# Optimization experiments

Measured on AMD Instinct MI355X. Metric: run time of the kernel, lower is better.

The kernel has to match this reference:

```python
import jax, jax.numpy as jnp
import numpy as np

HIDDEN = 2048
H = 16            # num heads
Q_RANK = 1536
KV_RANK = 512
D_NOPE = 128
D_ROPE = 64
D_QK = D_NOPE + D_ROPE   # 192
D_V = 128
ROPE_BASE = 10000.0
EPS = 1e-6


def _rms_norm(x, w):
    xf = x.astype(jnp.float32)
    var = jnp.mean(xf * xf, axis=-1, keepdims=True)
    return w * (xf * jax.lax.rsqrt(var + EPS)).astype(x.dtype)


def _rotate_half(x):
    x1, x2 = x[..., : x.shape[-1] // 2], x[..., x.shape[-1] // 2:]
    return jnp.concatenate((-x2, x1), axis=-1)


def _rope_cos_sin(position_ids, dtype):
    inv_freq = 1.0 / (ROPE_BASE ** (jnp.arange(0, D_ROPE, 2, dtype=jnp.float32) / D_ROPE))
    freqs = position_ids.astype(jnp.float32)[..., None] * inv_freq  # [b,s,32]
    emb = jnp.concatenate((freqs, freqs), axis=-1)                  # [b,s,64]
    return jnp.cos(emb).astype(dtype), jnp.sin(emb).astype(dtype)


def setup_inputs() -> dict:
    key = jax.random.key(0)
    ks = jax.random.split(key, 8)
    b, s = 1, 2048
    scale = 0.02
    return {
        "hidden_states": jax.random.normal(ks[0], (b, s, HIDDEN), jnp.float32),
        "position_ids": jnp.broadcast_to(jnp.arange(s, dtype=jnp.int64)[None, :], (b, s)),
        "q_a_w": jax.random.normal(ks[1], (Q_RANK, HIDDEN), jnp.float32) * scale,
        "q_a_ln_w": jnp.ones((Q_RANK,), jnp.float32),
        "q_b_w": jax.random.normal(ks[2], (H * D_QK, Q_RANK), jnp.float32) * scale,
        "kv_a_w": jax.random.normal(ks[3], (KV_RANK + D_ROPE, HIDDEN), jnp.float32) * scale,
        "kv_a_ln_w": jnp.ones((KV_RANK,), jnp.float32),
        "kv_b_w": jax.random.normal(ks[4], (H * (D_NOPE + D_V), KV_RANK), jnp.float32) * scale,
        "o_w": jax.random.normal(ks[5], (HIDDEN, H * D_V), jnp.float32) * scale,
    }


def reference(hidden_states, position_ids, q_a_w, q_a_ln_w, q_b_w, kv_a_w, kv_a_ln_w, kv_b_w, o_w):
    b, s, _ = hidden_states.shape
    softmax_scale = D_QK ** (-0.5)

    # Q path: low-rank down-proj -> RMSNorm -> up-proj
    q_a = hidden_states @ q_a_w.T                              # [b,s,q_rank]
    q = (_rms_norm(q_a, q_a_ln_w) @ q_b_w.T).reshape(b, s, H, D_QK)
    q_nope, q_pe = q[..., :D_NOPE], q[..., D_NOPE:]

    # KV path: joint down-proj -> split latent / rope part
    kv_a = hidden_states @ kv_a_w.T                            # [b,s,kv_rank+rope]
    compressed_kv = _rms_norm(kv_a[..., :KV_RANK], kv_a_ln_w)  # [b,s,kv_rank]
    k_pe = kv_a[..., KV_RANK:]                                 # [b,s,rope]
    kv_b = (compressed_kv @ kv_b_w.T).reshape(b, s, H, D_NOPE + D_V)
    k_nope, v = kv_b[..., :D_NOPE], kv_b[..., D_NOPE:]

    # decoupled RoPE on the rope slice
    cos, sin = _rope_cos_sin(position_ids, hidden_states.dtype)  # [b,s,64]
    cos, sin = cos[:, :, None, :], sin[:, :, None, :]            # [b,s,1,64]
    q_pe = q_pe * cos + _rotate_half(q_pe) * sin                 # [b,s,H,64]
    k_pe_h = jnp.broadcast_to(k_pe[:, :, None, :], (b, s, H, D_ROPE))
    k_pe_h = k_pe_h * cos + _rotate_half(k_pe_h) * sin

    q_full = jnp.concatenate([q_nope, q_pe], axis=-1)            # [b,s,H,192]
    k_full = jnp.concatenate([k_nope, k_pe_h], axis=-1)          # [b,s,H,192]

    # naive materialized attention (matches reference)
    scores = jnp.einsum("bqhd,bkhd->bhqk", q_full, k_full) * softmax_scale
    causal = jnp.triu(jnp.full((s, s), -jnp.inf, dtype=scores.dtype), k=1)
    scores = scores + causal
    probs = jax.nn.softmax(scores.astype(jnp.float32), axis=-1).astype(q_full.dtype)
    attn = jnp.einsum("bhqk,bkhd->bqhd", probs, v).reshape(b, s, H * D_V)
    return attn @ o_w.T
```

## Files before the change

kernel.cpp:

```cpp
#include <hip/hip_runtime.h>
#include <stdint.h>

#define S_LEN 2048
#define HIDDEN_ 2048
#define NH 16
#define QR 1536
#define KVR 512
#define DN 128
#define DR 64
#define DQK 192
#define DV 128

typedef __attribute__((ext_vector_type(8))) short bf16x8;
typedef __attribute__((ext_vector_type(4))) float f32x4;
typedef __attribute__((ext_vector_type(4))) unsigned short u16x4;
typedef unsigned short u16;
typedef unsigned int u32;

#define GLOAD_LDS16(g, l)                                                      \
    __builtin_amdgcn_global_load_lds(                                          \
        (const __attribute__((address_space(1))) void*)(g),                    \
        (__attribute__((address_space(3))) void*)(l), 16, 0, 0)

__device__ inline float bf2f(u16 x) {
    union { u32 u; float f; } v; v.u = ((u32)x) << 16; return v.f;
}
__device__ inline u16 f2bf(float f) {
    union { float f; u32 u; } v; v.f = f;
    u32 u = v.u;
    return (u16)((u + 0x7fffu + ((u >> 16) & 1u)) >> 16);
}

__global__ void cvt_multi(const float* s0, u16* d0, int n0,
                          const float* s1, u16* d1, int n1,
                          const float* s2, u16* d2, int n2,
                          const float* s3, u16* d3, int n3,
                          const float* s4, u16* d4, int n4,
                          const float* s5, u16* d5, int n5)
{
    const float* src; u16* dst; int n;
    switch (blockIdx.y) {
        case 0: src = s0; dst = d0; n = n0; break;
        case 1: src = s1; dst = d1; n = n1; break;
        case 2: src = s2; dst = d2; n = n2; break;
        case 3: src = s3; dst = d3; n = n3; break;
        case 4: src = s4; dst = d4; n = n4; break;
        default: src = s5; dst = d5; n = n5; break;
    }
    int i = (blockIdx.x * 256 + threadIdx.x) * 4;
    if (i + 3 < n) {
        float4 v = *(const float4*)(src + i);
        dst[i + 0] = f2bf(v.x);
        dst[i + 1] = f2bf(v.y);
        dst[i + 2] = f2bf(v.z);
        dst[i + 3] = f2bf(v.w);
    }
}

__global__ __launch_bounds__(256, 3)
void gemm_bt(const u16* __restrict__ A, const u16* __restrict__ B,
             void* __restrict__ Cv, int M, int N, int K, int out_f32)
{
    __shared__ u16 sA[128 * 32];
    __shared__ u16 sB[128 * 32];
    const int tid  = threadIdx.x;
    const int wave = tid >> 6;
    const int lane = tid & 63;
    const int l16  = lane & 15;
    const int quad = lane >> 4;
    const int m_blk = blockIdx.y * 128;
    const int n_blk = blockIdx.x * 128;
    const int wm = (wave >> 1) * 64;
    const int wn = (wave & 1) * 64;

    const f32x4 zero4 = {0.f, 0.f, 0.f, 0.f};
    f32x4 acc[4][4];
#pragma unroll
    for (int i = 0; i < 4; i++)
#pragma unroll
        for (int j = 0; j < 4; j++) acc[i][j] = zero4;

    const int srow = lane >> 2;
    const int scol = (lane & 3) * 8;

    for (int k0 = 0; k0 < K; k0 += 32) {
        __syncthreads();
#pragma unroll
        for (int p = 0; p < 2; p++) {
            const int rbase = wave * 32 + p * 16;
            const int row = rbase + srow;
            const u16* ga = A + (size_t)(m_blk + row) * K + k0 + scol;
            GLOAD_LDS16(ga, &sA[rbase * 32]);
            int brow = n_blk + row; if (brow >= N) brow = N - 1;
            const u16* gb = B + (size_t)brow * K + k0 + scol;
            GLOAD_LDS16(gb, &sB[rbase * 32]);
        }
        __syncthreads();

        bf16x8 af[4], bfr[4];
#pragma unroll
        for (int i = 0; i < 4; i++)
            af[i] = *(const bf16x8*)(sA + (wm + i * 16 + l16) * 32 + quad * 8);
#pragma unroll
        for (int j = 0; j < 4; j++)
            bfr[j] = *(const bf16x8*)(sB + (wn + j * 16 + l16) * 32 + quad * 8);
#pragma unroll
        for (int i = 0; i < 4; i++)
#pragma unroll
            for (int j = 0; j < 4; j++)
                acc[i][j] = __builtin_amdgcn_mfma_f32_16x16x32_bf16(
                    af[i], bfr[j], acc[i][j], 0, 0, 0);
    }

#pragma unroll
    for (int i = 0; i < 4; i++)
#pragma unroll
        for (int j = 0; j < 4; j++)
#pragma unroll
            for (int r = 0; r < 4; r++) {
                int mrow = m_blk + wm + i * 16 + quad * 4 + r;
                int ncol = n_blk + wn + j * 16 + l16;
                if (ncol < N) {
                    if (out_f32)
                        ((float*)Cv)[(size_t)mrow * N + ncol] = acc[i][j][r];
                    else
                        ((u16*)Cv)[(size_t)mrow * N + ncol] = f2bf(acc[i][j][r]);
                }
            }
}

__global__ void rmsnorm2_k(const u16* __restrict__ X0, const float* __restrict__ W0,
                           u16* __restrict__ Y0,
                           const u16* __restrict__ X1, const float* __restrict__ W1,
                           u16* __restrict__ Y1, int in_stride)
{
    const u16* X; const float* W; u16* Y; int len, out_stride;
    if (blockIdx.y == 0) { X = X0; W = W0; Y = Y0; len = QR;  out_stride = QR; }
    else                 { X = X1; W = W1; Y = Y1; len = KVR; out_stride = KVR; }
    const int row = blockIdx.x;
    const u16* x = X + (size_t)row * in_stride;
    u16* y = Y + (size_t)row * out_stride;
    float ss = 0.f;
    for (int i = threadIdx.x; i < len; i += 256) { float v = bf2f(x[i]); ss += v * v; }
#pragma unroll
    for (int off = 32; off; off >>= 1) ss += __shfl_down(ss, off, 64);
    __shared__ float red[4];
    if ((threadIdx.x & 63) == 0) red[threadIdx.x >> 6] = ss;
    __syncthreads();
    float tot = red[0] + red[1] + red[2] + red[3];
    float inv = 1.0f / sqrtf(tot / (float)len + 1e-6f);
    for (int i = threadIdx.x; i < len; i += 256)
        y[i] = f2bf(W[i] * bf2f(x[i]) * inv);
}

__global__ void rope_repack(const u16* __restrict__ q,
                            const u16* __restrict__ kvb,
                            const u16* __restrict__ kva_pe,
                            int kva_stride,
                            u16* __restrict__ Q, u16* __restrict__ Kf)
{
    const int s = blockIdx.x;
    const float pos = (float)s;
    const int t = threadIdx.x;
    __shared__ float cs[64], sn[64];
    __shared__ u16 kpe_r[64];
    if (t < 64) {
        int jf = t & 31;
        float freq = powf(10000.f, -(float)(2 * jf) / 64.f);
        float ang = pos * freq;
        cs[t] = cosf(ang);
        sn[t] = sinf(ang);
    }
    __syncthreads();
    if (t < 64) {
        int j = t;
        float x = bf2f(kva_pe[(size_t)s * kva_stride + j]);
        float other = (j < 32) ? -bf2f(kva_pe[(size_t)s * kva_stride + j + 32])
                               :  bf2f(kva_pe[(size_t)s * kva_stride + j - 32]);
        kpe_r[j] = f2bf(x * cs[j] + other * sn[j]);
    }
    __syncthreads();

    for (int idx = t; idx < NH * DQK; idx += 256) {
        int h = idx / DQK, d = idx % DQK;
        const size_t qrow = (size_t)s * (NH * DQK) + h * DQK;
        u16 qv;
        if (d < DN) qv = q[qrow + d];
        else {
            int j = d - DN;
            float x = bf2f(q[qrow + DN + j]);
            float other = (j < 32) ? -bf2f(q[qrow + DN + j + 32])
                                   :  bf2f(q[qrow + DN + j - 32]);
            qv = f2bf(x * cs[j] + other * sn[j]);
        }
        Q[((size_t)h * S_LEN + s) * DQK + d] = qv;
        u16 kv;
        if (d < DN) kv = kvb[(size_t)s * (NH * 256) + h * 256 + d];
        else        kv = kpe_r[d - DN];
        Kf[((size_t)h * S_LEN + s) * DQK + d] = kv;
    }
}

__global__ void transpose_v(const u16* __restrict__ kvb, u16* __restrict__ Vt)
{
    __shared__ u16 tile[64][72];
    const int h  = blockIdx.z;
    const int s0 = blockIdx.x * 64;
    const int d0 = blockIdx.y * 64;
    const int t  = threadIdx.x;
#pragma unroll
    for (int p = 0; p < 2; p++) {
        int c = p * 256 + t;
        int r = c >> 3, col = (c & 7) * 8;
        *(bf16x8*)&tile[r][col] =
            *(const bf16x8*)&kvb[(size_t)(s0 + r) * (NH * 256) + h * 256 + 128 + d0 + col];
    }
    __syncthreads();
#pragma unroll
    for (int p = 0; p < 2; p++) {
        int c = p * 256 + t;
        int dr = c >> 3, sc = (c & 7) * 8;
        bf16x8 v;
#pragma unroll
        for (int j = 0; j < 8; j++) v[j] = (short)tile[sc + j][dr];
        *(bf16x8*)&Vt[((size_t)h * DV + d0 + dr) * S_LEN + s0 + sc] = v;
    }
}

__global__ __launch_bounds__(256, 2)
void mla_attn(const u16* __restrict__ Q, const u16* __restrict__ Kf,
              const u16* __restrict__ Vt, u16* __restrict__ attn)
{
    const int h     = blockIdx.y;
    const int strip = (h < 8) ? blockIdx.x : (31 - blockIdx.x);
    const int wave  = threadIdx.x >> 6;
    const int lane  = threadIdx.x & 63;
    const int l16   = lane & 15;
    const int quad  = lane >> 4;
    const int q0    = strip * 64 + wave * 16;
    const int qrow  = q0 + l16;

    const u16* Qh  = Q  + (size_t)h * S_LEN * DQK;
    const u16* Kh  = Kf + (size_t)h * S_LEN * DQK;
    const u16* Vth = Vt + (size_t)h * DV * S_LEN;

    __shared__ u16 sK[2][24 * 32 * 8];
    __shared__ u16 sV[2][4 * 128 * 8];
    __shared__ u16 pbuf[4][16][36];
    u16 (*pb)[36] = pbuf[wave];

    bf16x8 qf[6];
#pragma unroll
    for (int st = 0; st < 6; st++)
        qf[st] = *(const bf16x8*)(Qh + (size_t)qrow * DQK + st * 32 + quad * 8);

    const f32x4 zero4 = {0.f, 0.f, 0.f, 0.f};
    f32x4 oacc[8];
#pragma unroll
    for (int t = 0; t < 8; t++) oacc[t] = zero4;
    float mrow = -INFINITY, lrow = 0.f;

    const float scale = 0.07216878364870323f;
    const int T = 2 * strip + 2;

    auto stage = [&](int buf, int c0) {
#pragma unroll
        for (int g = 0; g < 3; g++) {
            int c = g * 256 + wave * 64 + lane;
            int row = c & 31, cg = c >> 5;
            GLOAD_LDS16(Kh + (size_t)(c0 + row) * DQK + cg * 8,
                        &sK[buf][(g * 256 + wave * 64) * 8]);
        }
#pragma unroll
        for (int g = 0; g < 2; g++) {
            int c = g * 256 + wave * 64 + lane;
            int d = c & 127, cg = c >> 7;
            GLOAD_LDS16(Vth + (size_t)d * S_LEN + c0 + cg * 8,
                        &sV[buf][(g * 256 + wave * 64) * 8]);
        }
    };

    stage(0, 0);

    for (int kt = 0; kt < T; kt++) {
        const int c0  = kt * 32;
        const int cur = kt & 1;
        __syncthreads();
        if (kt + 1 < T) stage(cur ^ 1, c0 + 32);

        if (c0 <= q0 + 15) {
            f32x4 s0 = zero4, s1 = zero4;
#pragma unroll
            for (int st = 0; st < 6; st++) {
                bf16x8 k0 = *(const bf16x8*)&sK[cur][((st * 4 + quad) * 32 + l16) * 8];
                bf16x8 k1 = *(const bf16x8*)&sK[cur][((st * 4 + quad) * 32 + 16 + l16) * 8];
                s0 = __builtin_amdgcn_mfma_f32_16x16x32_bf16(k0, qf[st], s0, 0, 0, 0);
                s1 = __builtin_amdgcn_mfma_f32_16x16x32_bf16(k1, qf[st], s1, 0, 0, 0);
            }
            bf16x8 vfr[8];
#pragma unroll
            for (int t = 0; t < 8; t++)
                vfr[t] = *(const bf16x8*)&sV[cur][(quad * 128 + t * 16 + l16) * 8];

            const bool full = (c0 + 31 <= q0);
            float v0[4], v1[4];
#pragma unroll
            for (int r = 0; r < 4; r++) {
                v0[r] = s0[r] * scale;
                v1[r] = s1[r] * scale;
                if (!full) {
                    if (c0 + quad * 4 + r > qrow)      v0[r] = -INFINITY;
                    if (c0 + 16 + quad * 4 + r > qrow) v1[r] = -INFINITY;
                }
            }
            float lm = fmaxf(fmaxf(fmaxf(v0[0], v0[1]), fmaxf(v0[2], v0[3])),
                             fmaxf(fmaxf(v1[0], v1[1]), fmaxf(v1[2], v1[3])));
            lm = fmaxf(lm, __shfl_xor(lm, 16, 64));
            lm = fmaxf(lm, __shfl_xor(lm, 32, 64));
            const float mnew  = fmaxf(mrow, lm);
            const float alpha = __expf(mrow - mnew);
            float p0[4], p1[4], rs = 0.f;
#pragma unroll
            for (int r = 0; r < 4; r++) {
                p0[r] = __expf(v0[r] - mnew);
                p1[r] = __expf(v1[r] - mnew);
                rs += p0[r] + p1[r];
            }
            rs += __shfl_xor(rs, 16, 64);
            rs += __shfl_xor(rs, 32, 64);
            lrow = lrow * alpha + rs;
            mrow = mnew;
#pragma unroll
            for (int t = 0; t < 8; t++) oacc[t] *= alpha;

            u16x4 pk0, pk1;
#pragma unroll
            for (int r = 0; r < 4; r++) { pk0[r] = f2bf(p0[r]); pk1[r] = f2bf(p1[r]); }
            *(u16x4*)&pb[l16][quad * 4]      = pk0;
            *(u16x4*)&pb[l16][16 + quad * 4] = pk1;
            asm volatile("s_waitcnt lgkmcnt(0)" ::: "memory");
            bf16x8 pfrag = *(const bf16x8*)(&pb[l16][quad * 8]);

#pragma unroll
            for (int t = 0; t < 8; t++)
                oacc[t] = __builtin_amdgcn_mfma_f32_16x16x32_bf16(vfr[t], pfrag,
                                                                  oacc[t], 0, 0, 0);
        }
    }

    const float linv = 1.0f / lrow;
#pragma unroll
    for (int t = 0; t < 8; t++) {
        u16x4 ov;
#pragma unroll
        for (int r = 0; r < 4; r++) ov[r] = f2bf(oacc[t][r] * linv);
        *(u16x4*)&attn[(size_t)qrow * (NH * DV) + h * DV + t * 16 + quad * 4] = ov;
    }
}

extern "C" void kernel_launch(void* const* d_in, const int* in_sizes, int n_in,
                              void* d_out, int out_size, void* d_ws, size_t ws_size,
                              hipStream_t stream)
{
    const float* hid      = (const float*)d_in[0];
    const float* q_a_w    = (const float*)d_in[2];
    const float* q_a_ln_w = (const float*)d_in[3];
    const float* q_b_w    = (const float*)d_in[4];
    const float* kv_a_w   = (const float*)d_in[5];
    const float* kv_a_ln_w= (const float*)d_in[6];
    const float* kv_b_w   = (const float*)d_in[7];
    const float* o_w      = (const float*)d_in[8];

    const int NQKV = QR + KVR + DR;

    char* base = (char*)d_ws;
    u16* qkvaw_b = (u16*)(base + 0);
    u16* qbw_b   = (u16*)(base + 8650752);
    u16* kvbw_b  = (u16*)(base + 18087936);
    u16* ow_b    = (u16*)(base + 22282240);
    u16* hid_b   = (u16*)(base + 30670848);
    u16* qkv_a   = (u16*)(base + 39059456);
    u16* q_n     = (u16*)(base + 47710208);
    u16* ckv     = (u16*)(base + 54001664);
    u16* qb      = (u16*)(base + 56098816);
    u16* kvb     = (u16*)(base + 68681728);
    u16* Qb      = (u16*)(base + 85458944);
    u16* Kb      = (u16*)(base + 98041856);
    u16* Vtb     = (u16*)(base + 110624768);
    u16* attnb   = (u16*)(base + 39059456);

    cvt_multi<<<dim3(4608, 6), 256, 0, stream>>>(
        hid,    hid_b,                          HIDDEN_ * S_LEN,
        q_a_w,  qkvaw_b,                        QR * HIDDEN_,
        kv_a_w, qkvaw_b + (size_t)QR * HIDDEN_, (KVR + DR) * HIDDEN_,
        q_b_w,  qbw_b,                          NH * DQK * QR,
        kv_b_w, kvbw_b,                         NH * 256 * KVR,
        o_w,    ow_b,                           HIDDEN_ * NH * DV);

    gemm_bt<<<dim3((NQKV + 127) / 128, S_LEN / 128), 256, 0, stream>>>(
        hid_b, qkvaw_b, qkv_a, S_LEN, NQKV, HIDDEN_, 0);
    rmsnorm2_k<<<dim3(S_LEN, 2), 256, 0, stream>>>(
        qkv_a, q_a_ln_w, q_n, qkv_a + QR, kv_a_ln_w, ckv, NQKV);
    gemm_bt<<<dim3(NH * DQK / 128, S_LEN / 128), 256, 0, stream>>>(
        q_n, qbw_b, qb, S_LEN, NH * DQK, QR, 0);
    gemm_bt<<<dim3(NH * 256 / 128, S_LEN / 128), 256, 0, stream>>>(
        ckv, kvbw_b, kvb, S_LEN, NH * 256, KVR, 0);
    rope_repack<<<S_LEN, 256, 0, stream>>>(qb, kvb, qkv_a + QR + KVR, NQKV, Qb, Kb);
    transpose_v<<<dim3(S_LEN / 64, DV / 64, NH), 256, 0, stream>>>(kvb, Vtb);
    mla_attn<<<dim3(32, NH), 256, 0, stream>>>(Qb, Kb, Vtb, attnb);
    gemm_bt<<<dim3(HIDDEN_ / 128, S_LEN / 128), 256, 0, stream>>>(
        attnb, ow_b, (float*)d_out, S_LEN, HIDDEN_, HIDDEN_, 1);
}
```

Baseline: 402.5 us.

## Split long causal attention strips across two blocks and fuse the q_b/kv_b GEMMs

The attention kernel now splits each of the 16 longest query strips per head into two KV-range halves. Each half writes unnormalized partial outputs plus running max and sum to a float workspace, and a new combine kernel merges the halves with log-sum-exp weighting. This raises the grid from 512 to 768 blocks and shortens the longest per-block critical path. Separately, the q_b and kv_b up-projection GEMMs are merged into one launch using blockIdx.z, which removes a launch and lets the two fill the GPU together. The cost is an extra partials round trip through global memory, an extra small kernel, and some reuse of workspace space.

Measured after the change: 364.4 us. 9.5% less time.

```diff
diff --git a/kernel.cpp b/kernel.cpp
--- a/kernel.cpp
+++ b/kernel.cpp
@@ -57,9 +57,10 @@
     }
 }
 
-__global__ __launch_bounds__(256, 3)
-void gemm_bt(const u16* __restrict__ A, const u16* __restrict__ B,
-             void* __restrict__ Cv, int M, int N, int K, int out_f32)
+__device__ __forceinline__
+void gemm_body(const u16* __restrict__ A, const u16* __restrict__ B,
+               void* __restrict__ Cv, int M, int N, int K, int out_f32,
+               int bx, int by)
 {
     __shared__ u16 sA[128 * 32];
     __shared__ u16 sB[128 * 32];
@@ -68,8 +69,8 @@
     const int lane = tid & 63;
     const int l16  = lane & 15;
     const int quad = lane >> 4;
-    const int m_blk = blockIdx.y * 128;
-    const int n_blk = blockIdx.x * 128;
+    const int m_blk = by * 128;
+    const int n_blk = bx * 128;
     const int wm = (wave >> 1) * 64;
     const int wn = (wave & 1) * 64;
 
@@ -127,6 +128,25 @@
                         ((u16*)Cv)[(size_t)mrow * N + ncol] = f2bf(acc[i][j][r]);
                 }
             }
+}
+
+__global__ __launch_bounds__(256, 3)
+void gemm_bt(const u16* __restrict__ A, const u16* __restrict__ B,
+             void* __restrict__ Cv, int M, int N, int K, int out_f32)
+{
+    gemm_body(A, B, Cv, M, N, K, out_f32, blockIdx.x, blockIdx.y);
+}
+
+__global__ __launch_bounds__(256, 3)
+void gemm_dual(const u16* A0, const u16* B0, u16* C0, int M0, int N0, int K0,
+               const u16* A1, const u16* B1, u16* C1, int M1, int N1, int K1)
+{
+    if (blockIdx.z == 0) {
+        if ((int)blockIdx.x >= (N0 + 127) / 128) return;
+        gemm_body(A0, B0, C0, M0, N0, K0, 0, blockIdx.x, blockIdx.y);
+    } else {
+        gemm_body(A1, B1, C1, M1, N1, K1, 0, blockIdx.x, blockIdx.y);
+    }
 }
 
 __global__ void rmsnorm2_k(const u16* __restrict__ X0, const float* __restrict__ W0,
@@ -229,15 +249,21 @@
 
 __global__ __launch_bounds__(256, 2)
 void mla_attn(const u16* __restrict__ Q, const u16* __restrict__ Kf,
-              const u16* __restrict__ Vt, u16* __restrict__ attn)
-{
-    const int h     = blockIdx.y;
-    const int strip = (h < 8) ? blockIdx.x : (31 - blockIdx.x);
+              const u16* __restrict__ Vt, u16* __restrict__ attn,
+              float* __restrict__ part)
+{
+    const int h  = blockIdx.y;
+    const int bx = blockIdx.x;
+    int s, tb, te, cIdx; bool direct;
+    if (bx < 16)      { s = 16 + bx; tb = 0;  te = 32;        cIdx = 0; direct = false; }
+    else if (bx < 32) { s = 47 - bx; tb = 32; te = 2 * s + 2; cIdx = 1; direct = false; }
+    else              { s = 47 - bx; tb = 0;  te = 2 * s + 2; cIdx = 0; direct = true;  }
+
     const int wave  = threadIdx.x >> 6;
     const int lane  = threadIdx.x & 63;
     const int l16   = lane & 15;
     const int quad  = lane >> 4;
-    const int q0    = strip * 64 + wave * 16;
+    const int q0    = s * 64 + wave * 16;
     const int qrow  = q0 + l16;
 
     const u16* Qh  = Q  + (size_t)h * S_LEN * DQK;
@@ -261,7 +287,6 @@
     float mrow = -INFINITY, lrow = 0.f;
 
     const float scale = 0.07216878364870323f;
-    const int T = 2 * strip + 2;
 
     auto stage = [&](int buf, int c0) {
 #pragma unroll
@@ -280,13 +305,13 @@
         }
     };
 
-    stage(0, 0);
-
-    for (int kt = 0; kt < T; kt++) {
+    stage(0, tb * 32);
+
+    for (int kt = tb; kt < te; kt++) {
         const int c0  = kt * 32;
-        const int cur = kt & 1;
+        const int cur = (kt - tb) & 1;
         __syncthreads();
-        if (kt + 1 < T) stage(cur ^ 1, c0 + 32);
+        if (kt + 1 < te) stage(cur ^ 1, c0 + 32);
 
         if (c0 <= q0 + 15) {
             f32x4 s0 = zero4, s1 = zero4;
@@ -348,13 +373,44 @@
         }
     }
 
-    const float linv = 1.0f / lrow;
-#pragma unroll
-    for (int t = 0; t < 8; t++) {
-        u16x4 ov;
-#pragma unroll
-        for (int r = 0; r < 4; r++) ov[r] = f2bf(oacc[t][r] * linv);
-        *(u16x4*)&attn[(size_t)qrow * (NH * DV) + h * DV + t * 16 + quad * 4] = ov;
+    if (direct) {
+        const float linv = 1.0f / lrow;
+#pragma unroll
+        for (int t = 0; t < 8; t++) {
+            u16x4 ov;
+#pragma unroll
+            for (int r = 0; r < 4; r++) ov[r] = f2bf(oacc[t][r] * linv);
+            *(u16x4*)&attn[(size_t)qrow * (NH * DV) + h * DV + t * 16 + quad * 4] = ov;
+        }
+    } else {
+        float* pout = part + ((size_t)(h * 16 + (s - 16)) * 2 + cIdx) * 8320;
+        const int rowl = wave * 16 + l16;
+#pragma unroll
+        for (int t = 0; t < 8; t++) {
+            float4 ov = {oacc[t][0], oacc[t][1], oacc[t][2], oacc[t][3]};
+            *(float4*)&pout[(size_t)rowl * 128 + t * 16 + quad * 4] = ov;
+        }
+        if (quad == 0) {
+            pout[8192 + rowl] = mrow;
+            pout[8256 + rowl] = lrow;
+        }
+    }
+}
+
+__global__ void attn_combine(const float* __restrict__ part, u16* __restrict__ attn)
+{
+    const int h = blockIdx.y, sIdx = blockIdx.x;
+    const int s = 16 + sIdx;
+    const float* p0 = part + ((size_t)(h * 16 + sIdx) * 2 + 0) * 8320;
+    const float* p1 = p0 + 8320;
+    for (int e = threadIdx.x; e < 8192; e += 256) {
+        int row = e >> 7, d = e & 127;
+        float m0 = p0[8192 + row], m1 = p1[8192 + row];
+        float l0 = p0[8256 + row], l1 = p1[8256 + row];
+        float M  = fmaxf(m0, m1);
+        float w0 = __expf(m0 - M), w1 = __expf(m1 - M);
+        float o  = (w0 * p0[e] + w1 * p1[e]) / (w0 * l0 + w1 * l1);
+        attn[(size_t)(s * 64 + row) * (NH * DV) + h * DV + d] = f2bf(o);
     }
 }
 
@@ -388,6 +444,7 @@
     u16* Kb      = (u16*)(base + 98041856);
     u16* Vtb     = (u16*)(base + 110624768);
     u16* attnb   = (u16*)(base + 39059456);
+    float* partb = (float*)(base + 56098816);
 
     cvt_multi<<<dim3(4608, 6), 256, 0, stream>>>(
         hid,    hid_b,                          HIDDEN_ * S_LEN,
@@ -401,13 +458,13 @@
         hid_b, qkvaw_b, qkv_a, S_LEN, NQKV, HIDDEN_, 0);
     rmsnorm2_k<<<dim3(S_LEN, 2), 256, 0, stream>>>(
         qkv_a, q_a_ln_w, q_n, qkv_a + QR, kv_a_ln_w, ckv, NQKV);
-    gemm_bt<<<dim3(NH * DQK / 128, S_LEN / 128), 256, 0, stream>>>(
-        q_n, qbw_b, qb, S_LEN, NH * DQK, QR, 0);
-    gemm_bt<<<dim3(NH * 256 / 128, S_LEN / 128), 256, 0, stream>>>(
-        ckv, kvbw_b, kvb, S_LEN, NH * 256, KVR, 0);
+    gemm_dual<<<dim3(32, S_LEN / 128, 2), 256, 0, stream>>>(
+        q_n, qbw_b, qb,  S_LEN, NH * DQK, QR,
+        ckv, kvbw_b, kvb, S_LEN, NH * 256, KVR);
     rope_repack<<<S_LEN, 256, 0, stream>>>(qb, kvb, qkv_a + QR + KVR, NQKV, Qb, Kb);
     transpose_v<<<dim3(S_LEN / 64, DV / 64, NH), 256, 0, stream>>>(kvb, Vtb);
-    mla_attn<<<dim3(32, NH), 256, 0, stream>>>(Qb, Kb, Vtb, attnb);
+    mla_attn<<<dim3(48, NH), 256, 0, stream>>>(Qb, Kb, Vtb, attnb, partb);
+    attn_combine<<<dim3(16, NH), 256, 0, stream>>>(partb, attnb);
     gemm_bt<<<dim3(HIDDEN_ / 128, S_LEN / 128), 256, 0, stream>>>(
         attnb, ow_b, (float*)d_out, S_LEN, HIDDEN_, HIDDEN_, 1);
 }
```
